# Optimization experiments

Measured on AMD Instinct MI355X. Metric: run time of the kernel, lower is better.

The kernel has to match this reference:

```python
import jax, jax.numpy as jnp
import numpy as np

C_M, C_Z, C = 256, 128, 32
LN_EPS = 1e-5


def setup_inputs() -> dict:
    key = jax.random.key(0)
    ks = jax.random.split(key, 9)
    S, R = 128, 384  # N_seq, N_res
    m = jax.random.normal(ks[0], (S, R, C_M), dtype=jnp.float32)
    ln_g = jnp.ones((C_M,), jnp.float32)
    ln_b = jnp.zeros((C_M,), jnp.float32)
    w1 = jax.random.normal(ks[1], (C_M, C), jnp.float32) / np.sqrt(C_M)
    b1 = jnp.zeros((C,), jnp.float32)
    w2 = jax.random.normal(ks[2], (C_M, C), jnp.float32) / np.sqrt(C_M)
    b2 = jnp.zeros((C,), jnp.float32)
    w_out = jax.random.normal(ks[3], (C * C, C_Z), jnp.float32) / np.sqrt(C * C)
    b_out = jnp.zeros((C_Z,), jnp.float32)
    return {"m": m, "ln_g": ln_g, "ln_b": ln_b, "w1": w1, "b1": b1,
            "w2": w2, "b2": b2, "w_out": w_out, "b_out": b_out}


def reference(m, ln_g, ln_b, w1, b1, w2, b2, w_out, b_out):
    S, R, _ = m.shape
    # LayerNorm over c_m
    mu = jnp.mean(m, axis=-1, keepdims=True)
    var = jnp.var(m, axis=-1, keepdims=True)
    mn = (m - mu) * jax.lax.rsqrt(var + LN_EPS) * ln_g + ln_b
    a = mn @ w1 + b1  # (S, R, c)
    b = mn @ w2 + b2  # (S, R, c)
    # outer product summed over N_seq: out[i,j,x,y] = sum_s a[s,i,x] b[s,j,y]
    o = jnp.einsum('six,sjy->ijxy', a, b)  # (R, R, c, c)
    o = o.reshape(R, R, C * C) @ w_out + b_out  # (R, R, c_z)
    return o / S
```

## Files before the change

### kernel.cpp

```cpp
#include <hip/hip_runtime.h>
#include <hip/hip_bf16.h>

#define R_RES 384
#define S_SEQ 128
#define CM 256
#define CC 32
#define CZ 128

typedef __attribute__((ext_vector_type(8))) short bf16x8;
typedef __attribute__((ext_vector_type(4))) float f32x4;
typedef __attribute__((ext_vector_type(4))) int i32x4;

__device__ __forceinline__ short tobf16(float f) {
    union { __hip_bfloat16 h; short s; } u;
    u.h = __float2bfloat16(f);
    return u.s;
}

__device__ __forceinline__ void lgkm_barrier() {
    asm volatile("s_waitcnt lgkmcnt(0)" ::: "memory");
    __builtin_amdgcn_s_barrier();
    __builtin_amdgcn_sched_barrier(0);
}

__global__ void k_transpose_wout(const float* __restrict__ w_out, short* __restrict__ wbTf) {
    __shared__ float t[64][65];
    int k0 = blockIdx.x * 64;
    int z0 = blockIdx.y * 64;
    int tid = threadIdx.x;
    int c = tid & 63, rg = tid >> 6;
#pragma unroll
    for (int rr = 0; rr < 16; ++rr) {
        int kk = rg * 16 + rr;
        t[kk][c] = w_out[(size_t)(k0 + kk) * CZ + z0 + c];
    }
    __syncthreads();
#pragma unroll
    for (int l = 0; l < 2; ++l) {
        int id = l * 256 + tid;
        int f = id >> 6;
        int z16l = f >> 1, k32l = f & 1;
        int ln = id & 63;
        int zl = z16l * 16 + (ln & 15);
        int kl = k32l * 32 + (ln >> 4) * 8;
        bf16x8 pk;
#pragma unroll
        for (int j = 0; j < 8; ++j) pk[j] = tobf16(t[kl + j][zl]);
        int z16 = blockIdx.y * 4 + z16l;
        int k32 = blockIdx.x * 2 + k32l;
        *(bf16x8*)(wbTf + ((size_t)(z16 * 32 + k32) * 64 + ln) * 8) = pk;
    }
}

__global__ void k_pack_w12(const float* __restrict__ w1, const float* __restrict__ w2,
                           short* __restrict__ wcT) {
    int idx = blockIdx.x * 256 + threadIdx.x;
    int k = idx >> 6, n = idx & 63;
    float v = (n < 32) ? w1[k * CC + n] : w2[k * CC + (n - 32)];
    wcT[n * CM + k] = tobf16(v);
}

__global__ __launch_bounds__(256) void k_ln_proj(
    const float* __restrict__ M, const float* __restrict__ ln_g, const float* __restrict__ ln_b,
    const float* __restrict__ b1, const float* __restrict__ b2,
    const short* __restrict__ wcT, short* __restrict__ aTf, short* __restrict__ bTf) {
    __shared__ short mnb[64 * 256];
    __shared__ short ab_s[2][32 * 72];
    int r = blockIdx.x >> 1;
    int s0 = (blockIdx.x & 1) * 64;
    int tid = threadIdx.x, lane = tid & 63, w = tid >> 6;
    int g = lane >> 4, r16 = lane & 15;
    float4 gv = *(const float4*)(ln_g + lane * 4);
    float4 bv = *(const float4*)(ln_b + lane * 4);
    for (int it = 0; it < 16; ++it) {
        int sl = it * 4 + w;
        float4 v = *(const float4*)(M + ((size_t)(s0 + sl) * R_RES + r) * CM + lane * 4);
        float sum = v.x + v.y + v.z + v.w;
        float sq = v.x * v.x + v.y * v.y + v.z * v.z + v.w * v.w;
#pragma unroll
        for (int off = 32; off; off >>= 1) {
            sum += __shfl_xor(sum, off);
            sq  += __shfl_xor(sq, off);
        }
        float mu = sum * (1.0f / 256.0f);
        float var = sq * (1.0f / 256.0f) - mu * mu;
        float rstd = rsqrtf(var + 1e-5f);
        short4 mnp;
        mnp.x = tobf16((v.x - mu) * rstd * gv.x + bv.x);
        mnp.y = tobf16((v.y - mu) * rstd * gv.y + bv.y);
        mnp.z = tobf16((v.z - mu) * rstd * gv.z + bv.z);
        mnp.w = tobf16((v.w - mu) * rstd * gv.w + bv.w);
        int byte = sl * 512 + lane * 8;
        byte ^= ((sl & 7) << 4);
        *(short4*)((char*)mnb + byte) = mnp;
    }
    __syncthreads();
    f32x4 acc[4] = {{0,0,0,0},{0,0,0,0},{0,0,0,0},{0,0,0,0}};
    int srow = w * 16 + r16;
#pragma unroll
    for (int ks = 0; ks < 8; ++ks) {
        int byte = srow * 512 + ks * 64 + g * 16;
        byte ^= ((srow & 7) << 4);
        bf16x8 af = *(const bf16x8*)((const char*)mnb + byte);
#pragma unroll
        for (int nt = 0; nt < 4; ++nt) {
            bf16x8 bf = *(const bf16x8*)(wcT + (nt * 16 + r16) * CM + ks * 32 + g * 8);
            acc[nt] = __builtin_amdgcn_mfma_f32_16x16x32_bf16(af, bf, acc[nt], 0, 0, 0);
        }
    }
#pragma unroll
    for (int nt = 0; nt < 4; ++nt) {
        int n = nt * 16 + r16;
        int x = n & 31, sel = n >> 5;
        float bias = sel ? b2[x] : b1[x];
#pragma unroll
        for (int rr = 0; rr < 4; ++rr) {
            int sl = w * 16 + g * 4 + rr;
            ab_s[sel][x * 72 + sl] = tobf16(acc[nt][rr] + bias);
        }
    }
    __syncthreads();
    int piece = tid >> 6;
    int fl = piece >> 1, kl = piece & 1;
    int ln = tid & 63;
    int x = fl * 16 + (ln & 15);
    int s_loc = kl * 32 + (ln >> 4) * 8;
    i32x4 va = *(const i32x4*)((const char*)ab_s[0] + (x * 72 + s_loc) * 2);
    i32x4 vb = *(const i32x4*)((const char*)ab_s[1] + (x * 72 + s_loc) * 2);
    size_t off = ((((size_t)r * 2 + fl) * 4 + (s0 >> 5) + kl) * 64 + ln) * 16;
    *(i32x4*)((char*)aTf + off) = va;
    *(i32x4*)((char*)bTf + off) = vb;
}

__global__ __launch_bounds__(512, 2) void k_opm(
    const short* __restrict__ aTf, const short* __restrict__ bTf,
    const short* __restrict__ wbTf, const float* __restrict__ b_out,
    float* __restrict__ out) {
    __shared__ __align__(16) char smem[147456];
    int tid = threadIdx.x, lane = tid & 63, w = tid >> 6;
    int g = lane >> 4, r16 = lane & 15;
    int wm = w >> 1, wn = w & 1;
    int kh = w & 1, zq = w >> 1;

    int t0 = blockIdx.x * 36;
    const char* Ab = (const char*)aTf;
    const char* Bb = (const char*)bTf;

    {
        const char* gB0 = Bb + (size_t)(t0 % 96) * 32768;
        const char* gB1 = Bb + (size_t)((t0 + 1) % 96) * 32768;
#pragma unroll
        for (int q = 0; q < 4; ++q) {
            __builtin_amdgcn_global_load_lds(
                (const __attribute__((address_space(1))) void*)(gB0 + q * 8192 + tid * 16),
                (__attribute__((address_space(3))) void*)(smem + q * 8192 + tid * 16), 16, 0, 0);
            __builtin_amdgcn_global_load_lds(
                (const __attribute__((address_space(1))) void*)(gB1 + q * 8192 + tid * 16),
                (__attribute__((address_space(3))) void*)(smem + 32768 + q * 8192 + tid * 16), 16, 0, 0);
        }
    }
    bf16x8 wb[2][16];
#pragma unroll
    for (int zt = 0; zt < 2; ++zt)
#pragma unroll
        for (int ks2 = 0; ks2 < 16; ++ks2)
            wb[zt][ks2] = *(const bf16x8*)(wbTf +
                (((size_t)(zq * 2 + zt) * 32 + kh * 16 + ks2) * 64 + lane) * 8);

    int pR = tid >> 5;
    int zR = (tid & 31) * 4;
    float4 bo4 = *(const float4*)(b_out + zR);

    asm volatile("s_waitcnt vmcnt(0)" ::: "memory");
    __syncthreads();

    f32x4 acc[2][4] = {};
    {
        const char* gAc = Ab + (size_t)((t0 / 96) * 8 + wm * 2) * 4096;
#pragma unroll
        for (int ks = 0; ks < 4; ++ks) {
            bf16x8 afc0 = *(const bf16x8*)(gAc + ks * 1024 + lane * 16);
            bf16x8 afc1 = *(const bf16x8*)(gAc + 4096 + ks * 1024 + lane * 16);
            bf16x8 bf[4];
#pragma unroll
            for (int ni = 0; ni < 4; ++ni)
                bf[ni] = *(const bf16x8*)(smem + (((wn * 4 + ni) * 4 + ks) * 64 + lane) * 16);
            __builtin_amdgcn_s_setprio(1);
#pragma unroll
            for (int ni = 0; ni < 4; ++ni) {
                acc[0][ni] = __builtin_amdgcn_mfma_f32_16x16x32_bf16(bf[ni], afc0, acc[0][ni], 0, 0, 0);
                acc[1][ni] = __builtin_amdgcn_mfma_f32_16x16x32_bf16(bf[ni], afc1, acc[1][ni], 0, 0, 0);
            }
            __builtin_amdgcn_s_setprio(0);
        }
    }
    lgkm_barrier();
#pragma unroll
    for (int mi = 0; mi < 2; ++mi)
#pragma unroll
        for (int ni = 0; ni < 4; ++ni) {
            int p = wm * 4 + wn * 2 + (ni >> 1);
            int x = mi * 16 + r16;
            int y0 = (ni & 1) * 16 + g * 4;
            int byte = (p * 2048 + x * 64 + y0 * 2) ^ (((p & 7) ^ (x & 7)) << 4);
            short4 pk;
            pk.x = tobf16(acc[mi][ni][0]);
            pk.y = tobf16(acc[mi][ni][1]);
            pk.z = tobf16(acc[mi][ni][2]);
            pk.w = tobf16(acc[mi][ni][3]);
            *(short4*)(smem + 65536 + byte) = pk;
        }
    lgkm_barrier();

    for (int it = 0; it < 36; ++it) {
        int t = t0 + it;
        bool hasN = (it < 35);
        int tc = (it < 35) ? t + 1 : t;

        if (it < 34) {
            const char* gB = Bb + (size_t)((t + 2) % 96) * 32768;
            char* dst = smem + (it & 1) * 32768;
#pragma unroll
            for (int q = 0; q < 4; ++q)
                __builtin_amdgcn_global_load_lds(
                    (const __attribute__((address_space(1))) void*)(gB + q * 8192 + tid * 16),
                    (__attribute__((address_space(3))) void*)(dst + q * 8192 + tid * 16), 16, 0, 0);
        }

        const char* A2r = smem + 65536 + (it & 1) * 32768;
        const char* Bn  = smem + ((it + 1) & 1) * 32768;
        const char* gAc = Ab + (size_t)((tc / 96) * 8 + wm * 2) * 4096;

        f32x4 c0 = {0,0,0,0}, c1 = {0,0,0,0};
        f32x4 acc2[2][4] = {};
#pragma unroll
        for (int ks = 0; ks < 4; ++ks) {
            bf16x8 afc0, afc1, bf[4];
            if (hasN) {
                afc0 = *(const bf16x8*)(gAc + ks * 1024 + lane * 16);
                afc1 = *(const bf16x8*)(gAc + 4096 + ks * 1024 + lane * 16);
#pragma unroll
                for (int ni = 0; ni < 4; ++ni)
                    bf[ni] = *(const bf16x8*)(Bn + (((wn * 4 + ni) * 4 + ks) * 64 + lane) * 16);
            }
            bf16x8 a2f0, a2f1, a2f2, a2f3;
            {
                int x = kh * 16 + ks * 4 + 0;
                a2f0 = *(const bf16x8*)(A2r + ((r16 * 2048 + x * 64 + g * 16)
                        ^ ((((r16 & 7) ^ (x & 7))) << 4)));
                x = kh * 16 + ks * 4 + 1;
                a2f1 = *(const bf16x8*)(A2r + ((r16 * 2048 + x * 64 + g * 16)
                        ^ ((((r16 & 7) ^ (x & 7))) << 4)));
                x = kh * 16 + ks * 4 + 2;
                a2f2 = *(const bf16x8*)(A2r + ((r16 * 2048 + x * 64 + g * 16)
                        ^ ((((r16 & 7) ^ (x & 7))) << 4)));
                x = kh * 16 + ks * 4 + 3;
                a2f3 = *(const bf16x8*)(A2r + ((r16 * 2048 + x * 64 + g * 16)
                        ^ ((((r16 & 7) ^ (x & 7))) << 4)));
            }
            __builtin_amdgcn_s_setprio(1);
            c0 = __builtin_amdgcn_mfma_f32_16x16x32_bf16(wb[0][ks * 4 + 0], a2f0, c0, 0, 0, 0);
            c1 = __builtin_amdgcn_mfma_f32_16x16x32_bf16(wb[1][ks * 4 + 0], a2f0, c1, 0, 0, 0);
            c0 = __builtin_amdgcn_mfma_f32_16x16x32_bf16(wb[0][ks * 4 + 1], a2f1, c0, 0, 0, 0);
            c1 = __builtin_amdgcn_mfma_f32_16x16x32_bf16(wb[1][ks * 4 + 1], a2f1, c1, 0, 0, 0);
            if (hasN) {
#pragma unroll
                for (int ni = 0; ni < 4; ++ni)
                    acc2[0][ni] = __builtin_amdgcn_mfma_f32_16x16x32_bf16(bf[ni], afc0, acc2[0][ni], 0, 0, 0);
            }
            c0 = __builtin_amdgcn_mfma_f32_16x16x32_bf16(wb[0][ks * 4 + 2], a2f2, c0, 0, 0, 0);
            c1 = __builtin_amdgcn_mfma_f32_16x16x32_bf16(wb[1][ks * 4 + 2], a2f2, c1, 0, 0, 0);
            c0 = __builtin_amdgcn_mfma_f32_16x16x32_bf16(wb[0][ks * 4 + 3], a2f3, c0, 0, 0, 0);
            c1 = __builtin_amdgcn_mfma_f32_16x16x32_bf16(wb[1][ks * 4 + 3], a2f3, c1, 0, 0, 0);
            if (hasN) {
#pragma unroll
                for (int ni = 0; ni < 4; ++ni)
                    acc2[1][ni] = __builtin_amdgcn_mfma_f32_16x16x32_bf16(bf[ni], afc1, acc2[1][ni], 0, 0, 0);
            }
            __builtin_amdgcn_s_setprio(0);
        }

        {
            int b0 = (kh * 8192 + r16 * 512 + (zq * 32 + g * 4) * 4) ^ ((r16 & 7) << 4);
            int b1 = (kh * 8192 + r16 * 512 + (zq * 32 + 16 + g * 4) * 4) ^ ((r16 & 7) << 4);
            *(f32x4*)(smem + 131072 + b0) = c0;
            *(f32x4*)(smem + 131072 + b1) = c1;
        }
        lgkm_barrier();

        if (hasN) {
            char* A2w = smem + 65536 + ((it + 1) & 1) * 32768;
#pragma unroll
            for (int mi = 0; mi < 2; ++mi)
#pragma unroll
                for (int ni = 0; ni < 4; ++ni) {
                    int p = wm * 4 + wn * 2 + (ni >> 1);
                    int x = mi * 16 + r16;
                    int y0 = (ni & 1) * 16 + g * 4;
                    int byte = (p * 2048 + x * 64 + y0 * 2) ^ (((p & 7) ^ (x & 7)) << 4);
                    short4 pk;
                    pk.x = tobf16(acc2[mi][ni][0]);
                    pk.y = tobf16(acc2[mi][ni][1]);
                    pk.z = tobf16(acc2[mi][ni][2]);
                    pk.w = tobf16(acc2[mi][ni][3]);
                    *(short4*)(A2w + byte) = pk;
                }
        }

        {
            int base = (pR * 512 + zR * 4) ^ ((pR & 7) << 4);
            f32x4 v0 = *(const f32x4*)(smem + 131072 + base);
            f32x4 v1 = *(const f32x4*)(smem + 131072 + 8192 + base);
            f32x4 res;
            res[0] = (v0[0] + v1[0] + bo4.x) * (1.0f / 128.0f);
            res[1] = (v0[1] + v1[1] + bo4.y) * (1.0f / 128.0f);
            res[2] = (v0[2] + v1[2] + bo4.z) * (1.0f / 128.0f);
            res[3] = (v0[3] + v1[3] + bo4.w) * (1.0f / 128.0f);
            int bi4 = t / 96, bj4 = t % 96;
            int ig = bi4 * 4 + (pR >> 2);
            int jg = bj4 * 4 + (pR & 3);
            *(f32x4*)(out + ((size_t)ig * R_RES + jg) * CZ + zR) = res;
        }

        asm volatile("s_waitcnt vmcnt(0)" ::: "memory");
        __syncthreads();
    }
}

extern "C" void kernel_launch(void* const* d_in, const int* in_sizes, int n_in,
                              void* d_out, int out_size, void* d_ws, size_t ws_size,
                              hipStream_t stream) {
    const float* M     = (const float*)d_in[0];
    const float* ln_g  = (const float*)d_in[1];
    const float* ln_b  = (const float*)d_in[2];
    const float* w1    = (const float*)d_in[3];
    const float* b1    = (const float*)d_in[4];
    const float* w2    = (const float*)d_in[5];
    const float* b2    = (const float*)d_in[6];
    const float* w_out = (const float*)d_in[7];
    const float* b_out = (const float*)d_in[8];
    float* out = (float*)d_out;

    short* aTf  = (short*)d_ws;
    short* bTf  = aTf + 12288 * 128;
    short* wbTf = bTf + 12288 * 128;
    short* wcT  = wbTf + 128 * 1024;

    k_transpose_wout<<<dim3(16, 2), 256, 0, stream>>>(w_out, wbTf);
    k_pack_w12<<<64, 256, 0, stream>>>(w1, w2, wcT);
    k_ln_proj<<<768, 256, 0, stream>>>(M, ln_g, ln_b, b1, b2, wcT, aTf, bTf);
    k_opm<<<256, 512, 0, stream>>>(aTf, bTf, wbTf, b_out, out);
}
```

Baseline: 118.4 us.

## Repartition output GEMM over full K per wave to drop LDS reduction

Each wave now owns 16 output channels over the full K=1024 reduction instead of 32 channels over half of K. The partial sums no longer need to be exchanged and added through LDS. This removes the LDS staging buffer (16KB), one block barrier per tile and the LDS stores and loads of the partial sums, and the epilogue writes directly from the accumulators. In exchange each wave holds 32 weight fragments in registers, and the two accumulators form a dependent MFMA chain over a longer K loop. The smaller shared memory footprint may also help residency.

New measurement: 117.9 us. About the same (-0.4%).

```diff
diff --git a/kernel.cpp b/kernel.cpp
--- a/kernel.cpp
+++ b/kernel.cpp
@@ -136,11 +136,10 @@
     const short* __restrict__ aTf, const short* __restrict__ bTf,
     const short* __restrict__ wbTf, const float* __restrict__ b_out,
     float* __restrict__ out) {
-    __shared__ __align__(16) char smem[147456];
+    __shared__ __align__(16) char smem[131072];
     int tid = threadIdx.x, lane = tid & 63, w = tid >> 6;
     int g = lane >> 4, r16 = lane & 15;
     int wm = w >> 1, wn = w & 1;
-    int kh = w & 1, zq = w >> 1;
 
     int t0 = blockIdx.x * 36;
     const char* Ab = (const char*)aTf;
@@ -159,17 +158,13 @@
                 (__attribute__((address_space(3))) void*)(smem + 32768 + q * 8192 + tid * 16), 16, 0, 0);
         }
     }
-    bf16x8 wb[2][16];
-#pragma unroll
-    for (int zt = 0; zt < 2; ++zt)
-#pragma unroll
-        for (int ks2 = 0; ks2 < 16; ++ks2)
-            wb[zt][ks2] = *(const bf16x8*)(wbTf +
-                (((size_t)(zq * 2 + zt) * 32 + kh * 16 + ks2) * 64 + lane) * 8);
-
-    int pR = tid >> 5;
-    int zR = (tid & 31) * 4;
-    float4 bo4 = *(const float4*)(b_out + zR);
+    bf16x8 wb[32];
+#pragma unroll
+    for (int k32 = 0; k32 < 32; ++k32)
+        wb[k32] = *(const bf16x8*)(wbTf + (((size_t)w * 32 + k32) * 64 + lane) * 8);
+
+    int zb = w * 16 + g * 4;
+    float4 bo4 = *(const float4*)(b_out + zb);
 
     asm volatile("s_waitcnt vmcnt(0)" ::: "memory");
     __syncthreads();
@@ -212,10 +207,13 @@
         }
     lgkm_barrier();
 
+    int abase = r16 * 2048 + g * 16;
+    int akey = (r16 & 7) << 4;
+
     for (int it = 0; it < 36; ++it) {
         int t = t0 + it;
         bool hasN = (it < 35);
-        int tc = (it < 35) ? t + 1 : t;
+        int tc = hasN ? t + 1 : t;
 
         if (it < 34) {
             const char* gB = Bb + (size_t)((t + 2) % 96) * 32768;
@@ -234,59 +232,34 @@
         f32x4 c0 = {0,0,0,0}, c1 = {0,0,0,0};
         f32x4 acc2[2][4] = {};
 #pragma unroll
-        for (int ks = 0; ks < 4; ++ks) {
+        for (int kq = 0; kq < 8; ++kq) {
+            bf16x8 a2f0 = *(const bf16x8*)(A2r + ((abase + (kq * 4 + 0) * 64) ^ (akey ^ ((((kq * 4 + 0) & 7)) << 4))));
+            bf16x8 a2f1 = *(const bf16x8*)(A2r + ((abase + (kq * 4 + 1) * 64) ^ (akey ^ ((((kq * 4 + 1) & 7)) << 4))));
+            bf16x8 a2f2 = *(const bf16x8*)(A2r + ((abase + (kq * 4 + 2) * 64) ^ (akey ^ ((((kq * 4 + 2) & 7)) << 4))));
+            bf16x8 a2f3 = *(const bf16x8*)(A2r + ((abase + (kq * 4 + 3) * 64) ^ (akey ^ ((((kq * 4 + 3) & 7)) << 4))));
             bf16x8 afc0, afc1, bf[4];
-            if (hasN) {
-                afc0 = *(const bf16x8*)(gAc + ks * 1024 + lane * 16);
-                afc1 = *(const bf16x8*)(gAc + 4096 + ks * 1024 + lane * 16);
+            if (hasN && kq < 4) {
+                afc0 = *(const bf16x8*)(gAc + kq * 1024 + lane * 16);
+                afc1 = *(const bf16x8*)(gAc + 4096 + kq * 1024 + lane * 16);
 #pragma unroll
                 for (int ni = 0; ni < 4; ++ni)
-                    bf[ni] = *(const bf16x8*)(Bn + (((wn * 4 + ni) * 4 + ks) * 64 + lane) * 16);
-            }
-            bf16x8 a2f0, a2f1, a2f2, a2f3;
-            {
-                int x = kh * 16 + ks * 4 + 0;
-                a2f0 = *(const bf16x8*)(A2r + ((r16 * 2048 + x * 64 + g * 16)
-                        ^ ((((r16 & 7) ^ (x & 7))) << 4)));
-                x = kh * 16 + ks * 4 + 1;
-                a2f1 = *(const bf16x8*)(A2r + ((r16 * 2048 + x * 64 + g * 16)
-                        ^ ((((r16 & 7) ^ (x & 7))) << 4)));
-                x = kh * 16 + ks * 4 + 2;
-                a2f2 = *(const bf16x8*)(A2r + ((r16 * 2048 + x * 64 + g * 16)
-                        ^ ((((r16 & 7) ^ (x & 7))) << 4)));
-                x = kh * 16 + ks * 4 + 3;
-                a2f3 = *(const bf16x8*)(A2r + ((r16 * 2048 + x * 64 + g * 16)
-                        ^ ((((r16 & 7) ^ (x & 7))) << 4)));
+                    bf[ni] = *(const bf16x8*)(Bn + (((wn * 4 + ni) * 4 + kq) * 64 + lane) * 16);
             }
             __builtin_amdgcn_s_setprio(1);
-            c0 = __builtin_amdgcn_mfma_f32_16x16x32_bf16(wb[0][ks * 4 + 0], a2f0, c0, 0, 0, 0);
-            c1 = __builtin_amdgcn_mfma_f32_16x16x32_bf16(wb[1][ks * 4 + 0], a2f0, c1, 0, 0, 0);
-            c0 = __builtin_amdgcn_mfma_f32_16x16x32_bf16(wb[0][ks * 4 + 1], a2f1, c0, 0, 0, 0);
-            c1 = __builtin_amdgcn_mfma_f32_16x16x32_bf16(wb[1][ks * 4 + 1], a2f1, c1, 0, 0, 0);
-            if (hasN) {
+            c0 = __builtin_amdgcn_mfma_f32_16x16x32_bf16(wb[kq * 4 + 0], a2f0, c0, 0, 0, 0);
+            c1 = __builtin_amdgcn_mfma_f32_16x16x32_bf16(wb[kq * 4 + 1], a2f1, c1, 0, 0, 0);
+            c0 = __builtin_amdgcn_mfma_f32_16x16x32_bf16(wb[kq * 4 + 2], a2f2, c0, 0, 0, 0);
+            c1 = __builtin_amdgcn_mfma_f32_16x16x32_bf16(wb[kq * 4 + 3], a2f3, c1, 0, 0, 0);
+            if (hasN && kq < 4) {
 #pragma unroll
                 for (int ni = 0; ni < 4; ++ni)
                     acc2[0][ni] = __builtin_amdgcn_mfma_f32_16x16x32_bf16(bf[ni], afc0, acc2[0][ni], 0, 0, 0);
-            }
-            c0 = __builtin_amdgcn_mfma_f32_16x16x32_bf16(wb[0][ks * 4 + 2], a2f2, c0, 0, 0, 0);
-            c1 = __builtin_amdgcn_mfma_f32_16x16x32_bf16(wb[1][ks * 4 + 2], a2f2, c1, 0, 0, 0);
-            c0 = __builtin_amdgcn_mfma_f32_16x16x32_bf16(wb[0][ks * 4 + 3], a2f3, c0, 0, 0, 0);
-            c1 = __builtin_amdgcn_mfma_f32_16x16x32_bf16(wb[1][ks * 4 + 3], a2f3, c1, 0, 0, 0);
-            if (hasN) {
 #pragma unroll
                 for (int ni = 0; ni < 4; ++ni)
                     acc2[1][ni] = __builtin_amdgcn_mfma_f32_16x16x32_bf16(bf[ni], afc1, acc2[1][ni], 0, 0, 0);
             }
             __builtin_amdgcn_s_setprio(0);
         }
-
-        {
-            int b0 = (kh * 8192 + r16 * 512 + (zq * 32 + g * 4) * 4) ^ ((r16 & 7) << 4);
-            int b1 = (kh * 8192 + r16 * 512 + (zq * 32 + 16 + g * 4) * 4) ^ ((r16 & 7) << 4);
-            *(f32x4*)(smem + 131072 + b0) = c0;
-            *(f32x4*)(smem + 131072 + b1) = c1;
-        }
-        lgkm_barrier();
 
         if (hasN) {
             char* A2w = smem + 65536 + ((it + 1) & 1) * 32768;
@@ -308,18 +281,15 @@
         }
 
         {
-            int base = (pR * 512 + zR * 4) ^ ((pR & 7) << 4);
-            f32x4 v0 = *(const f32x4*)(smem + 131072 + base);
-            f32x4 v1 = *(const f32x4*)(smem + 131072 + 8192 + base);
+            int bi4 = t / 96, bj4 = t % 96;
+            int ig = bi4 * 4 + (r16 >> 2);
+            int jg = bj4 * 4 + (r16 & 3);
             f32x4 res;
-            res[0] = (v0[0] + v1[0] + bo4.x) * (1.0f / 128.0f);
-            res[1] = (v0[1] + v1[1] + bo4.y) * (1.0f / 128.0f);
-            res[2] = (v0[2] + v1[2] + bo4.z) * (1.0f / 128.0f);
-            res[3] = (v0[3] + v1[3] + bo4.w) * (1.0f / 128.0f);
-            int bi4 = t / 96, bj4 = t % 96;
-            int ig = bi4 * 4 + (pR >> 2);
-            int jg = bj4 * 4 + (pR & 3);
-            *(f32x4*)(out + ((size_t)ig * R_RES + jg) * CZ + zR) = res;
+            res[0] = (c0[0] + c1[0] + bo4.x) * (1.0f / 128.0f);
+            res[1] = (c0[1] + c1[1] + bo4.y) * (1.0f / 128.0f);
+            res[2] = (c0[2] + c1[2] + bo4.z) * (1.0f / 128.0f);
+            res[3] = (c0[3] + c1[3] + bo4.w) * (1.0f / 128.0f);
+            *(f32x4*)(out + ((size_t)ig * R_RES + jg) * CZ + zb) = res;
         }
 
         asm volatile("s_waitcnt vmcnt(0)" ::: "memory");
```
